# Kernel tuning notes

Measured on AMD Instinct MI355X. Metric: run time of the kernel, lower is better.

The kernel has to match this reference:

```python
import jax, jax.numpy as jnp
import numpy as np
from jax import lax

B, S, H, W = 64, 256, 512, 512


def _lstm_cell(x_t, h, c, Wih, Whh, bih, bhh):
    # PyTorch LSTMCell gate order: i, f, g, o
    g = x_t @ Wih.T + h @ Whh.T + bih + bhh  # [B, 4H]
    i, f, gg, o = jnp.split(g, 4, axis=-1)
    c_new = jax.nn.sigmoid(f) * c + jax.nn.sigmoid(i) * jnp.tanh(gg)
    h_new = jax.nn.sigmoid(o) * jnp.tanh(c_new)
    return h_new, c_new


def setup_inputs() -> dict:
    key = jax.random.key(0)
    ks = jax.random.split(key, 12)
    bnd = 1.0 / np.sqrt(H)
    u = lambda k, shape, b: jax.random.uniform(k, shape, jnp.float32, -b, b)
    return {
        "x": jax.random.normal(ks[0], (B, S, S), jnp.float32),
        "enc_Wih": u(ks[1], (4 * H, S), bnd),
        "enc_Whh": u(ks[2], (4 * H, H), bnd),
        "enc_bih": u(ks[3], (4 * H,), bnd),
        "enc_bhh": u(ks[4], (4 * H,), bnd),
        "dec_Wih": u(ks[5], (4 * H, S), bnd),
        "dec_Whh": u(ks[6], (4 * H, H), bnd),
        "dec_bih": u(ks[7], (4 * H,), bnd),
        "dec_bhh": u(ks[8], (4 * H,), bnd),
        "w1": u(ks[9], (W, H), 1.0 / np.sqrt(H)),
        "w2": u(ks[10], (W, H), 1.0 / np.sqrt(H)),
        "vt": u(ks[11], (W,), 1.0 / np.sqrt(W)),
    }


def reference(x, enc_Wih, enc_Whh, enc_bih, enc_bhh,
              dec_Wih, dec_Whh, dec_bih, dec_bhh, w1, w2, vt):
    xs = x.transpose(1, 0, 2)  # [S, B, S] time-major

    # ---- encoder LSTM (zero initial state, PyTorch default) ----
    def enc_step(carry, x_t):
        h, c = carry
        h, c = _lstm_cell(x_t, h, c, enc_Wih, enc_Whh, enc_bih, enc_bhh)
        return (h, c), h

    h0 = jnp.zeros((B, H), x.dtype)
    (hT, cT), enc_out = lax.scan(enc_step, (h0, h0), xs)  # enc_out: [S, B, H]

    # loop-invariant W1 projection of encoder outputs
    e1 = jnp.einsum('sbh,wh->sbw', enc_out, w1)  # [S, B, W]

    # ---- decoder: hidden updates each step; cell stays at cT (faithful to source) ----
    def dec_step(h, x_t):
        h_new, _ = _lstm_cell(x_t, h, cT, dec_Wih, dec_Whh, dec_bih, dec_bhh)
        att = jnp.tanh(e1 + (h_new @ w2.T)[None, :, :])   # [S, B, W]
        scores = jnp.einsum('sbw,w->sb', att, vt)          # [S, B]
        lp = jax.nn.log_softmax(scores.T, axis=-1)         # [B, S]
        return h_new, lp

    _, probs = lax.scan(dec_step, hT, xs)  # [S_dec, B, S]
    return probs.transpose(1, 0, 2)        # [B, S_dec, S]
```

## Files before the change

kernel.cpp:

```cpp
#include <hip/hip_runtime.h>
#include <cmath>

__device__ __forceinline__ float sigm(float x) { return 1.0f / (1.0f + __expf(-x)); }

__global__ __launch_bounds__(256) void transpose_w(const float* __restrict__ in,
                                                   float* __restrict__ outT, int K) {
  __shared__ float tile[32][33];
  int tx = threadIdx.x & 31, ty = threadIdx.x >> 5;
  int k0 = blockIdx.x * 32;
  int j0 = blockIdx.y * 32;
#pragma unroll
  for (int i = 0; i < 32; i += 8)
    tile[ty + i][tx] = in[(size_t)(j0 + ty + i) * K + k0 + tx];
  __syncthreads();
#pragma unroll
  for (int i = 0; i < 32; i += 8)
    outT[(size_t)(k0 + ty + i) * 2048 + j0 + tx] = tile[tx][ty + i];
}

__global__ __launch_bounds__(256, 1) void lstm_chain(
    const float* __restrict__ WT, const float* __restrict__ x,
    const float* __restrict__ bih, const float* __restrict__ bhh,
    float* __restrict__ HBUF,
    float* __restrict__ Cst,
    unsigned int* __restrict__ cnt,
    int is_enc) {
  extern __shared__ float lds[];
  float4* W4 = (float4*)lds;
  float4* A4 = (float4*)(lds + 24576);
  float* gates = lds + 24576 + 12288;
  const int bg = blockIdx.x >> 6, ng = blockIdx.x & 63;
  const int tid = threadIdx.x;
  unsigned int* arr = cnt + bg * 128;
  unsigned int* rel = cnt + bg * 128 + 64;

#pragma unroll
  for (int r = 0; r < 24; ++r) {
    int idx = tid + 256 * r;
    int k = idx >> 3, j = idx & 7;
    float4 v =
        *(const float4*)(WT + (size_t)k * 2048 + (j >> 1) * 512 + ng * 8 + (j & 1) * 4);
    W4[k * 8 + (j ^ ((k >> 2) & 7))] = v;
  }
  float bi_i = 0.f, bi_f = 0.f, bi_g = 0.f, bi_o = 0.f, creg = 0.f;
  if (tid < 128) {
    int b = tid >> 3, n8 = tid & 7;
    int n_g = ng * 8 + n8;
    bi_i = bih[n_g] + bhh[n_g];
    bi_f = bih[512 + n_g] + bhh[512 + n_g];
    bi_g = bih[1024 + n_g] + bhh[1024 + n_g];
    bi_o = bih[1536 + n_g] + bhh[1536 + n_g];
    if (!is_enc) creg = Cst[(size_t)(bg * 16 + b) * 512 + n_g];
  }
#pragma unroll
  for (int r = 0; r < 8; ++r) {
    int idx = tid + 256 * r;
    int b = idx >> 7, q = idx & 127;
    float4 v;
    if (is_enc)
      v = make_float4(0.f, 0.f, 0.f, 0.f);
    else
      v = *(const float4*)(HBUF + ((size_t)(255 * 64) + bg * 16 + b) * 512 + 4 * q);
    A4[b * 192 + (q ^ ((b >> 1) & 7))] = v;
  }
#pragma unroll
  for (int r = 0; r < 4; ++r) {
    int idx = tid + 256 * r;
    int b = idx >> 6, q = idx & 63;
    float4 v = *(const float4*)(x + ((size_t)(bg * 16 + b) * 256 + 0) * 256 + 4 * q);
    A4[b * 192 + ((128 + q) ^ ((b >> 1) & 7))] = v;
  }
  __syncthreads();

  const int w = tid >> 6;
  const int lane = tid & 63;
  const int kq = lane >> 3, b8 = lane & 7;
  const int b0 = 2 * b8, b1 = b0 + 1;
  const int jlo = (2 * w) ^ kq, jhi = (2 * w + 1) ^ kq;
  const int kqx = kq ^ b8;

  for (int t = 0; t < 256; ++t) {
    float acc0[8], acc1[8];
#pragma unroll
    for (int g = 0; g < 8; ++g) { acc0[g] = 0.f; acc1[g] = 0.f; }
#pragma unroll 2
    for (int j = 0; j < 24; ++j) {
      int qa = (j << 3) + kqx;
      float4 a0 = A4[b0 * 192 + qa];
      float4 a1 = A4[b1 * 192 + qa];
      int wr = ((j << 3) + kq) << 2;
      float a0v[4] = {a0.x, a0.y, a0.z, a0.w};
      float a1v[4] = {a1.x, a1.y, a1.z, a1.w};
#pragma unroll
      for (int i = 0; i < 4; ++i) {
        float4 wlo = W4[(wr + i) * 8 + jlo];
        float4 whi = W4[(wr + i) * 8 + jhi];
        acc0[0] = fmaf(a0v[i], wlo.x, acc0[0]);
        acc0[1] = fmaf(a0v[i], wlo.y, acc0[1]);
        acc0[2] = fmaf(a0v[i], wlo.z, acc0[2]);
        acc0[3] = fmaf(a0v[i], wlo.w, acc0[3]);
        acc0[4] = fmaf(a0v[i], whi.x, acc0[4]);
        acc0[5] = fmaf(a0v[i], whi.y, acc0[5]);
        acc0[6] = fmaf(a0v[i], whi.z, acc0[6]);
        acc0[7] = fmaf(a0v[i], whi.w, acc0[7]);
        acc1[0] = fmaf(a1v[i], wlo.x, acc1[0]);
        acc1[1] = fmaf(a1v[i], wlo.y, acc1[1]);
        acc1[2] = fmaf(a1v[i], wlo.z, acc1[2]);
        acc1[3] = fmaf(a1v[i], wlo.w, acc1[3]);
        acc1[4] = fmaf(a1v[i], whi.x, acc1[4]);
        acc1[5] = fmaf(a1v[i], whi.y, acc1[5]);
        acc1[6] = fmaf(a1v[i], whi.z, acc1[6]);
        acc1[7] = fmaf(a1v[i], whi.w, acc1[7]);
      }
    }
#pragma unroll
    for (int d = 8; d <= 32; d <<= 1) {
#pragma unroll
      for (int g = 0; g < 8; ++g) {
        acc0[g] += __shfl_xor(acc0[g], d, 64);
        acc1[g] += __shfl_xor(acc1[g], d, 64);
      }
    }
    if (kq == 0) {
#pragma unroll
      for (int g = 0; g < 8; ++g) {
        gates[b0 * 40 + w * 8 + g] = acc0[g];
        gates[b1 * 40 + w * 8 + g] = acc1[g];
      }
    }
    __syncthreads();
    if (tid < 128) {
      int b = tid >> 3, n8 = tid & 7;
      float pi = gates[b * 40 + n8] + bi_i;
      float pf = gates[b * 40 + 8 + n8] + bi_f;
      float pg = gates[b * 40 + 16 + n8] + bi_g;
      float po = gates[b * 40 + 24 + n8] + bi_o;
      float ig = sigm(pi), fg = sigm(pf), gg = tanhf(pg), og = sigm(po);
      float cn = fmaf(fg, creg, ig * gg);
      if (is_enc) creg = cn;
      float hn = og * tanhf(cn);
      float* hp = HBUF + ((size_t)t * 64 + bg * 16 + b) * 512 + ng * 8 + n8;
      __hip_atomic_store(hp, hn, __ATOMIC_RELAXED, __HIP_MEMORY_SCOPE_AGENT);
      if (is_enc && t == 255) Cst[(size_t)(bg * 16 + b) * 512 + ng * 8 + n8] = cn;
    }
    if (t < 255) {
      asm volatile("s_waitcnt vmcnt(0)" ::: "memory");
      __syncthreads();
      unsigned old = 0;
      const unsigned tgt = 64u * (unsigned)(t + 1);
      if (tid == 0)
        old = __hip_atomic_fetch_add(arr, 1u, __ATOMIC_RELAXED,
                                     __HIP_MEMORY_SCOPE_AGENT);
#pragma unroll
      for (int r = 0; r < 4; ++r) {
        int idx = tid + 256 * r;
        int b = idx >> 6, q = idx & 63;
        float4 v =
            *(const float4*)(x + ((size_t)(bg * 16 + b) * 256 + (t + 1)) * 256 + 4 * q);
        A4[b * 192 + ((128 + q) ^ ((b >> 1) & 7))] = v;
      }
      if (tid == 0) {
        if (old == tgt - 1u) {
          __hip_atomic_store(rel, tgt, __ATOMIC_RELAXED, __HIP_MEMORY_SCOPE_AGENT);
        } else {
          while (__hip_atomic_load(rel, __ATOMIC_RELAXED, __HIP_MEMORY_SCOPE_AGENT) <
                 tgt)
            __builtin_amdgcn_s_sleep(1);
        }
      }
      __syncthreads();
      const float4* hb = (const float4*)(HBUF + (size_t)t * 64 * 512);
#pragma unroll
      for (int r = 0; r < 8; ++r) {
        int idx = tid + 256 * r;
        int b = idx >> 7, q = idx & 127;
        float4 v = hb[(size_t)(bg * 16 + b) * 128 + q];
        A4[b * 192 + (q ^ ((b >> 1) & 7))] = v;
      }
      __syncthreads();
    }
  }
}

__global__ __launch_bounds__(256) void gemm_fp32(const float* __restrict__ A,
                                                 const float* __restrict__ W,
                                                 float* __restrict__ C, int N, int K) {
  __shared__ float As[16 * 132];
  __shared__ float Ws[16 * 132];
  int tid = threadIdx.x;
  int n0 = blockIdx.x * 128, m0 = blockIdx.y * 128;
  int row = tid >> 1;
  int kbase = (tid & 1) * 8;
  const float* ap = A + (size_t)(m0 + row) * K;
  const float* wp = W + (size_t)(n0 + row) * K;
  int ty = tid >> 4, tx = tid & 15;
  float acc[8][8];
#pragma unroll
  for (int i = 0; i < 8; ++i)
#pragma unroll
    for (int j = 0; j < 8; ++j) acc[i][j] = 0.f;

  for (int kt = 0; kt < K; kt += 16) {
    float4 va0 = *(const float4*)(ap + kt + kbase);
    float4 va1 = *(const float4*)(ap + kt + kbase + 4);
    float4 vw0 = *(const float4*)(wp + kt + kbase);
    float4 vw1 = *(const float4*)(wp + kt + kbase + 4);
    __syncthreads();
    As[(kbase + 0) * 132 + row] = va0.x;
    As[(kbase + 1) * 132 + row] = va0.y;
    As[(kbase + 2) * 132 + row] = va0.z;
    As[(kbase + 3) * 132 + row] = va0.w;
    As[(kbase + 4) * 132 + row] = va1.x;
    As[(kbase + 5) * 132 + row] = va1.y;
    As[(kbase + 6) * 132 + row] = va1.z;
    As[(kbase + 7) * 132 + row] = va1.w;
    Ws[(kbase + 0) * 132 + row] = vw0.x;
    Ws[(kbase + 1) * 132 + row] = vw0.y;
    Ws[(kbase + 2) * 132 + row] = vw0.z;
    Ws[(kbase + 3) * 132 + row] = vw0.w;
    Ws[(kbase + 4) * 132 + row] = vw1.x;
    Ws[(kbase + 5) * 132 + row] = vw1.y;
    Ws[(kbase + 6) * 132 + row] = vw1.z;
    Ws[(kbase + 7) * 132 + row] = vw1.w;
    __syncthreads();
#pragma unroll
    for (int kk = 0; kk < 16; ++kk) {
      float4 a0 = *(const float4*)&As[kk * 132 + ty * 8];
      float4 a1 = *(const float4*)&As[kk * 132 + ty * 8 + 4];
      float4 w0 = *(const float4*)&Ws[kk * 132 + tx * 8];
      float4 w1 = *(const float4*)&Ws[kk * 132 + tx * 8 + 4];
      float av[8] = {a0.x, a0.y, a0.z, a0.w, a1.x, a1.y, a1.z, a1.w};
      float wv[8] = {w0.x, w0.y, w0.z, w0.w, w1.x, w1.y, w1.z, w1.w};
#pragma unroll
      for (int i = 0; i < 8; ++i)
#pragma unroll
        for (int j = 0; j < 8; ++j) acc[i][j] = fmaf(av[i], wv[j], acc[i][j]);
    }
  }
#pragma unroll
  for (int i = 0; i < 8; ++i) {
    float* cp = C + (size_t)(m0 + ty * 8 + i) * N + n0 + tx * 8;
    *(float4*)cp = make_float4(acc[i][0], acc[i][1], acc[i][2], acc[i][3]);
    *(float4*)(cp + 4) = make_float4(acc[i][4], acc[i][5], acc[i][6], acc[i][7]);
  }
}

__global__ __launch_bounds__(128) void scorer(const float* __restrict__ E1,
                                              const float* __restrict__ H2,
                                              const float* __restrict__ vt,
                                              float* __restrict__ out) {
  __shared__ float e1s[8 * 516];
  __shared__ float h2s[16 * 516];
  int tid = threadIdx.x;
  int sx = blockIdx.x;
  int b = blockIdx.y;
#pragma unroll
  for (int j = 0; j < 8; ++j) {
    int idx = tid + 128 * j;
    int r = idx >> 7, c4 = idx & 127;
    float4 v = *(const float4*)(E1 + ((size_t)(sx * 8 + r) * 64 + b) * 512 + c4 * 4);
    *(float4*)&e1s[r * 516 + c4 * 4] = v;
  }
  int tl = tid >> 3, sl = tid & 7;
  for (int tt = 0; tt < 16; ++tt) {
    __syncthreads();
#pragma unroll
    for (int j = 0; j < 16; ++j) {
      int idx = tid + 128 * j;
      int r = idx >> 7, c4 = idx & 127;
      float4 v = *(const float4*)(H2 + ((size_t)(tt * 16 + r) * 64 + b) * 512 + c4 * 4);
      *(float4*)&h2s[r * 516 + c4 * 4] = v;
    }
    __syncthreads();
    float acc = 0.f;
    const float* ep = &e1s[sl * 516];
    const float* hp = &h2s[tl * 516];
#pragma unroll 8
    for (int w4 = 0; w4 < 128; ++w4) {
      float4 a = *(const float4*)(ep + w4 * 4);
      float4 h = *(const float4*)(hp + w4 * 4);
      float4 vv = *(const float4*)(vt + w4 * 4);
      float x0 = a.x + h.x, x1 = a.y + h.y, x2 = a.z + h.z, x3 = a.w + h.w;
      float t0 = fmaf(-2.f, __builtin_amdgcn_rcpf(__expf(x0 + x0) + 1.f), 1.f);
      float t1 = fmaf(-2.f, __builtin_amdgcn_rcpf(__expf(x1 + x1) + 1.f), 1.f);
      float t2 = fmaf(-2.f, __builtin_amdgcn_rcpf(__expf(x2 + x2) + 1.f), 1.f);
      float t3 = fmaf(-2.f, __builtin_amdgcn_rcpf(__expf(x3 + x3) + 1.f), 1.f);
      acc = fmaf(t0, vv.x, acc);
      acc = fmaf(t1, vv.y, acc);
      acc = fmaf(t2, vv.z, acc);
      acc = fmaf(t3, vv.w, acc);
    }
    out[((size_t)b * 256 + tt * 16 + tl) * 256 + sx * 8 + sl] = acc;
  }
}

__global__ __launch_bounds__(256) void logsoftmax_kernel(float* __restrict__ out) {
  __shared__ float red[256];
  int tid = threadIdx.x;
  float* row = out + (size_t)blockIdx.x * 256;
  float v = row[tid];
  red[tid] = v;
  __syncthreads();
  for (int off = 128; off > 0; off >>= 1) {
    if (tid < off) red[tid] = fmaxf(red[tid], red[tid + off]);
    __syncthreads();
  }
  float mx = red[0];
  __syncthreads();
  red[tid] = __expf(v - mx);
  __syncthreads();
  for (int off = 128; off > 0; off >>= 1) {
    if (tid < off) red[tid] += red[tid + off];
    __syncthreads();
  }
  float lse = logf(red[0]);
  row[tid] = v - mx - lse;
}

extern "C" void kernel_launch(void* const* d_in, const int* in_sizes, int n_in,
                              void* d_out, int out_size, void* d_ws, size_t ws_size,
                              hipStream_t stream) {
  (void)in_sizes; (void)n_in; (void)out_size; (void)ws_size;
  const float* x = (const float*)d_in[0];
  const float* eWih = (const float*)d_in[1];
  const float* eWhh = (const float*)d_in[2];
  const float* ebih = (const float*)d_in[3];
  const float* ebhh = (const float*)d_in[4];
  const float* dWih = (const float*)d_in[5];
  const float* dWhh = (const float*)d_in[6];
  const float* dbih = (const float*)d_in[7];
  const float* dbhh = (const float*)d_in[8];
  const float* w1 = (const float*)d_in[9];
  const float* w2 = (const float*)d_in[10];
  const float* vt = (const float*)d_in[11];
  float* out = (float*)d_out;
  float* ws = (float*)d_ws;

  float* E1 = ws;
  float* H2 = E1 + 8388608ull;
  float* HBUF = H2 + 8388608ull;
  float* WTe = HBUF + 8388608ull;
  float* WTd = WTe + 1572864ull;
  float* Cst = WTd + 1572864ull;
  unsigned int* CNT = (unsigned int*)(Cst + 32768ull);

  const unsigned ldsB = (24576 + 12288 + 640) * 4;

  hipMemsetAsync(CNT, 0, 1024 * sizeof(unsigned int), stream);
  transpose_w<<<dim3(16, 64), 256, 0, stream>>>(eWhh, WTe, 512);
  transpose_w<<<dim3(8, 64), 256, 0, stream>>>(eWih, WTe + 512 * 2048, 256);
  transpose_w<<<dim3(16, 64), 256, 0, stream>>>(dWhh, WTd, 512);
  transpose_w<<<dim3(8, 64), 256, 0, stream>>>(dWih, WTd + 512 * 2048, 256);

  {
    const float* a0 = WTe; const float* a1 = x; const float* a2 = ebih;
    const float* a3 = ebhh; float* a4 = HBUF; float* a5 = Cst;
    unsigned int* a6 = CNT; int a7 = 1;
    void* args[] = {&a0, &a1, &a2, &a3, &a4, &a5, &a6, &a7};
    hipLaunchCooperativeKernel((const void*)lstm_chain, dim3(256), dim3(256), args,
                               ldsB, stream);
  }
  gemm_fp32<<<dim3(4, 128), 256, 0, stream>>>(HBUF, w1, E1, 512, 512);
  {
    const float* a0 = WTd; const float* a1 = x; const float* a2 = dbih;
    const float* a3 = dbhh; float* a4 = HBUF; float* a5 = Cst;
    unsigned int* a6 = CNT + 512; int a7 = 0;
    void* args[] = {&a0, &a1, &a2, &a3, &a4, &a5, &a6, &a7};
    hipLaunchCooperativeKernel((const void*)lstm_chain, dim3(256), dim3(256), args,
                               ldsB, stream);
  }
  gemm_fp32<<<dim3(4, 128), 256, 0, stream>>>(HBUF, w2, H2, 512, 512);
  scorer<<<dim3(32, 64), 128, 0, stream>>>(E1, H2, vt, out);
  logsoftmax_kernel<<<16384, 256, 0, stream>>>(out);
}
```

Measured before the change: 4.715 ms.

## Replace counter barrier with per-block flags and enlarge scorer tiles

After: 4.029 ms. 14.5% less time.

```diff
diff --git a/kernel.cpp b/kernel.cpp
--- a/kernel.cpp
+++ b/kernel.cpp
@@ -18,12 +18,45 @@
     outT[(size_t)(k0 + ty + i) * 2048 + j0 + tx] = tile[tx][ty + i];
 }
 
+__device__ __forceinline__ void gemv_j(const float4* __restrict__ A4,
+                                       const float4* __restrict__ W4, int j, int kqx,
+                                       int kq, int jlo, int jhi, int b0, int b1,
+                                       float (&o0)[8], float (&o1)[8]) {
+  int qa = (j << 3) + kqx;
+  float4 a04 = A4[b0 * 192 + qa];
+  float4 a14 = A4[b1 * 192 + qa];
+  int wr = ((j << 3) + kq) << 2;
+  float a0v[4] = {a04.x, a04.y, a04.z, a04.w};
+  float a1v[4] = {a14.x, a14.y, a14.z, a14.w};
+#pragma unroll
+  for (int i = 0; i < 4; ++i) {
+    float4 wlo = W4[(wr + i) * 8 + jlo];
+    float4 whi = W4[(wr + i) * 8 + jhi];
+    o0[0] = fmaf(a0v[i], wlo.x, o0[0]);
+    o0[1] = fmaf(a0v[i], wlo.y, o0[1]);
+    o0[2] = fmaf(a0v[i], wlo.z, o0[2]);
+    o0[3] = fmaf(a0v[i], wlo.w, o0[3]);
+    o0[4] = fmaf(a0v[i], whi.x, o0[4]);
+    o0[5] = fmaf(a0v[i], whi.y, o0[5]);
+    o0[6] = fmaf(a0v[i], whi.z, o0[6]);
+    o0[7] = fmaf(a0v[i], whi.w, o0[7]);
+    o1[0] = fmaf(a1v[i], wlo.x, o1[0]);
+    o1[1] = fmaf(a1v[i], wlo.y, o1[1]);
+    o1[2] = fmaf(a1v[i], wlo.z, o1[2]);
+    o1[3] = fmaf(a1v[i], wlo.w, o1[3]);
+    o1[4] = fmaf(a1v[i], whi.x, o1[4]);
+    o1[5] = fmaf(a1v[i], whi.y, o1[5]);
+    o1[6] = fmaf(a1v[i], whi.z, o1[6]);
+    o1[7] = fmaf(a1v[i], whi.w, o1[7]);
+  }
+}
+
 __global__ __launch_bounds__(256, 1) void lstm_chain(
     const float* __restrict__ WT, const float* __restrict__ x,
     const float* __restrict__ bih, const float* __restrict__ bhh,
     float* __restrict__ HBUF,
     float* __restrict__ Cst,
-    unsigned int* __restrict__ cnt,
+    unsigned int* __restrict__ flg,
     int is_enc) {
   extern __shared__ float lds[];
   float4* W4 = (float4*)lds;
@@ -31,8 +64,8 @@
   float* gates = lds + 24576 + 12288;
   const int bg = blockIdx.x >> 6, ng = blockIdx.x & 63;
   const int tid = threadIdx.x;
-  unsigned int* arr = cnt + bg * 128;
-  unsigned int* rel = cnt + bg * 128 + 64;
+  unsigned int* myflag = flg + (size_t)(bg * 64 + ng) * 32;
+  unsigned int* dom = flg + (size_t)bg * 64 * 32;
 
 #pragma unroll
   for (int r = 0; r < 24; ++r) {
@@ -84,35 +117,8 @@
 #pragma unroll
     for (int g = 0; g < 8; ++g) { acc0[g] = 0.f; acc1[g] = 0.f; }
 #pragma unroll 2
-    for (int j = 0; j < 24; ++j) {
-      int qa = (j << 3) + kqx;
-      float4 a0 = A4[b0 * 192 + qa];
-      float4 a1 = A4[b1 * 192 + qa];
-      int wr = ((j << 3) + kq) << 2;
-      float a0v[4] = {a0.x, a0.y, a0.z, a0.w};
-      float a1v[4] = {a1.x, a1.y, a1.z, a1.w};
-#pragma unroll
-      for (int i = 0; i < 4; ++i) {
-        float4 wlo = W4[(wr + i) * 8 + jlo];
-        float4 whi = W4[(wr + i) * 8 + jhi];
-        acc0[0] = fmaf(a0v[i], wlo.x, acc0[0]);
-        acc0[1] = fmaf(a0v[i], wlo.y, acc0[1]);
-        acc0[2] = fmaf(a0v[i], wlo.z, acc0[2]);
-        acc0[3] = fmaf(a0v[i], wlo.w, acc0[3]);
-        acc0[4] = fmaf(a0v[i], whi.x, acc0[4]);
-        acc0[5] = fmaf(a0v[i], whi.y, acc0[5]);
-        acc0[6] = fmaf(a0v[i], whi.z, acc0[6]);
-        acc0[7] = fmaf(a0v[i], whi.w, acc0[7]);
-        acc1[0] = fmaf(a1v[i], wlo.x, acc1[0]);
-        acc1[1] = fmaf(a1v[i], wlo.y, acc1[1]);
-        acc1[2] = fmaf(a1v[i], wlo.z, acc1[2]);
-        acc1[3] = fmaf(a1v[i], wlo.w, acc1[3]);
-        acc1[4] = fmaf(a1v[i], whi.x, acc1[4]);
-        acc1[5] = fmaf(a1v[i], whi.y, acc1[5]);
-        acc1[6] = fmaf(a1v[i], whi.z, acc1[6]);
-        acc1[7] = fmaf(a1v[i], whi.w, acc1[7]);
-      }
-    }
+    for (int j = 0; j < 24; ++j)
+      gemv_j(A4, W4, j, kqx, kq, jlo, jhi, b0, b1, acc0, acc1);
 #pragma unroll
     for (int d = 8; d <= 32; d <<= 1) {
 #pragma unroll
@@ -143,42 +149,40 @@
       __hip_atomic_store(hp, hn, __ATOMIC_RELAXED, __HIP_MEMORY_SCOPE_AGENT);
       if (is_enc && t == 255) Cst[(size_t)(bg * 16 + b) * 512 + ng * 8 + n8] = cn;
     }
-    if (t < 255) {
-      asm volatile("s_waitcnt vmcnt(0)" ::: "memory");
-      __syncthreads();
-      unsigned old = 0;
-      const unsigned tgt = 64u * (unsigned)(t + 1);
-      if (tid == 0)
-        old = __hip_atomic_fetch_add(arr, 1u, __ATOMIC_RELAXED,
-                                     __HIP_MEMORY_SCOPE_AGENT);
-#pragma unroll
-      for (int r = 0; r < 4; ++r) {
-        int idx = tid + 256 * r;
-        int b = idx >> 6, q = idx & 63;
-        float4 v =
-            *(const float4*)(x + ((size_t)(bg * 16 + b) * 256 + (t + 1)) * 256 + 4 * q);
-        A4[b * 192 + ((128 + q) ^ ((b >> 1) & 7))] = v;
+    if (t == 255) break;
+    asm volatile("s_waitcnt vmcnt(0)" ::: "memory");
+    __syncthreads();
+    if (tid == 0)
+      __hip_atomic_store(myflag, (unsigned)(t + 1), __ATOMIC_RELAXED,
+                         __HIP_MEMORY_SCOPE_AGENT);
+    asm volatile("" ::: "memory");
+#pragma unroll
+    for (int r = 0; r < 4; ++r) {
+      int idx = tid + 256 * r;
+      int b = idx >> 6, q = idx & 63;
+      float4 v =
+          *(const float4*)(x + ((size_t)(bg * 16 + b) * 256 + (t + 1)) * 256 + 4 * q);
+      A4[b * 192 + ((128 + q) ^ ((b >> 1) & 7))] = v;
+    }
+    if (tid < 64) {
+      const unsigned tgt = (unsigned)(t + 1);
+      unsigned int* fp = dom + (size_t)tid * 32;
+      while (true) {
+        unsigned v = __hip_atomic_load(fp, __ATOMIC_RELAXED, __HIP_MEMORY_SCOPE_AGENT);
+        if (__all((int)(v >= tgt))) break;
+        __builtin_amdgcn_s_sleep(1);
       }
-      if (tid == 0) {
-        if (old == tgt - 1u) {
-          __hip_atomic_store(rel, tgt, __ATOMIC_RELAXED, __HIP_MEMORY_SCOPE_AGENT);
-        } else {
-          while (__hip_atomic_load(rel, __ATOMIC_RELAXED, __HIP_MEMORY_SCOPE_AGENT) <
-                 tgt)
-            __builtin_amdgcn_s_sleep(1);
-        }
-      }
-      __syncthreads();
-      const float4* hb = (const float4*)(HBUF + (size_t)t * 64 * 512);
-#pragma unroll
-      for (int r = 0; r < 8; ++r) {
-        int idx = tid + 256 * r;
-        int b = idx >> 7, q = idx & 127;
-        float4 v = hb[(size_t)(bg * 16 + b) * 128 + q];
-        A4[b * 192 + (q ^ ((b >> 1) & 7))] = v;
-      }
-      __syncthreads();
-    }
+    }
+    __syncthreads();
+    const float4* hb = (const float4*)(HBUF + (size_t)t * 64 * 512);
+#pragma unroll
+    for (int r = 0; r < 8; ++r) {
+      int idx = tid + 256 * r;
+      int b = idx >> 7, q = idx & 127;
+      float4 v = hb[(size_t)(bg * 16 + b) * 128 + q];
+      A4[b * 192 + (q ^ ((b >> 1) & 7))] = v;
+    }
+    __syncthreads();
   }
 }
 
@@ -245,28 +249,29 @@
   }
 }
 
-__global__ __launch_bounds__(128) void scorer(const float* __restrict__ E1,
+__global__ __launch_bounds__(256) void scorer(const float* __restrict__ E1,
                                               const float* __restrict__ H2,
                                               const float* __restrict__ vt,
                                               float* __restrict__ out) {
-  __shared__ float e1s[8 * 516];
-  __shared__ float h2s[16 * 516];
+  extern __shared__ float smem[];
+  float* e1s = smem;
+  float* h2s = smem + 8256;
   int tid = threadIdx.x;
   int sx = blockIdx.x;
   int b = blockIdx.y;
 #pragma unroll
   for (int j = 0; j < 8; ++j) {
-    int idx = tid + 128 * j;
+    int idx = tid + 256 * j;
     int r = idx >> 7, c4 = idx & 127;
-    float4 v = *(const float4*)(E1 + ((size_t)(sx * 8 + r) * 64 + b) * 512 + c4 * 4);
+    float4 v = *(const float4*)(E1 + ((size_t)(sx * 16 + r) * 64 + b) * 512 + c4 * 4);
     *(float4*)&e1s[r * 516 + c4 * 4] = v;
   }
-  int tl = tid >> 3, sl = tid & 7;
+  int tl = tid >> 4, sl = tid & 15;
   for (int tt = 0; tt < 16; ++tt) {
     __syncthreads();
 #pragma unroll
-    for (int j = 0; j < 16; ++j) {
-      int idx = tid + 128 * j;
+    for (int j = 0; j < 8; ++j) {
+      int idx = tid + 256 * j;
       int r = idx >> 7, c4 = idx & 127;
       float4 v = *(const float4*)(H2 + ((size_t)(tt * 16 + r) * 64 + b) * 512 + c4 * 4);
       *(float4*)&h2s[r * 516 + c4 * 4] = v;
@@ -290,7 +295,7 @@
       acc = fmaf(t2, vv.z, acc);
       acc = fmaf(t3, vv.w, acc);
     }
-    out[((size_t)b * 256 + tt * 16 + tl) * 256 + sx * 8 + sl] = acc;
+    out[((size_t)b * 256 + tt * 16 + tl) * 256 + sx * 16 + sl] = acc;
   }
 }
 
@@ -342,11 +347,12 @@
   float* WTe = HBUF + 8388608ull;
   float* WTd = WTe + 1572864ull;
   float* Cst = WTd + 1572864ull;
-  unsigned int* CNT = (unsigned int*)(Cst + 32768ull);
+  unsigned int* FLG = (unsigned int*)(Cst + 32768ull);
 
   const unsigned ldsB = (24576 + 12288 + 640) * 4;
-
-  hipMemsetAsync(CNT, 0, 1024 * sizeof(unsigned int), stream);
+  const unsigned scorerLds = 2 * 16 * 516 * 4;
+
+  hipMemsetAsync(FLG, 0, 16384 * sizeof(unsigned int), stream);
   transpose_w<<<dim3(16, 64), 256, 0, stream>>>(eWhh, WTe, 512);
   transpose_w<<<dim3(8, 64), 256, 0, stream>>>(eWih, WTe + 512 * 2048, 256);
   transpose_w<<<dim3(16, 64), 256, 0, stream>>>(dWhh, WTd, 512);
@@ -355,7 +361,7 @@
   {
     const float* a0 = WTe; const float* a1 = x; const float* a2 = ebih;
     const float* a3 = ebhh; float* a4 = HBUF; float* a5 = Cst;
-    unsigned int* a6 = CNT; int a7 = 1;
+    unsigned int* a6 = FLG; int a7 = 1;
     void* args[] = {&a0, &a1, &a2, &a3, &a4, &a5, &a6, &a7};
     hipLaunchCooperativeKernel((const void*)lstm_chain, dim3(256), dim3(256), args,
                                ldsB, stream);
@@ -364,12 +370,12 @@
   {
     const float* a0 = WTd; const float* a1 = x; const float* a2 = dbih;
     const float* a3 = dbhh; float* a4 = HBUF; float* a5 = Cst;
-    unsigned int* a6 = CNT + 512; int a7 = 0;
+    unsigned int* a6 = FLG + 8192; int a7 = 0;
     void* args[] = {&a0, &a1, &a2, &a3, &a4, &a5, &a6, &a7};
     hipLaunchCooperativeKernel((const void*)lstm_chain, dim3(256), dim3(256), args,
                                ldsB, stream);
   }
   gemm_fp32<<<dim3(4, 128), 256, 0, stream>>>(HBUF, w2, H2, 512, 512);
-  scorer<<<dim3(32, 64), 128, 0, stream>>>(E1, H2, vt, out);
+  scorer<<<dim3(16, 64), 256, scorerLds, stream>>>(E1, H2, vt, out);
   logsoftmax_kernel<<<16384, 256, 0, stream>>>(out);
 }
```
